# Optimization experiments

Measured on AMD Instinct MI355X. Metric: run time of the kernel, lower is better.

## Reference

```python
import jax, jax.numpy as jnp
import numpy as np

# LIFNode defaults from spikingjelly: decay_input=True, hard reset (v_reset=0.0),
# surrogate = Sigmoid(alpha=4.0).
TAU = 2.0
V_TH = 0.1
V_RESET = 0.0
ALPHA = 4.0  # sigmoid surrogate sharpness

@jax.custom_vjp
def heaviside(x):
    return (x >= 0).astype(x.dtype)

def _hv_fwd(x):
    return heaviside(x), x

def _hv_bwd(x, g):
    s = jax.nn.sigmoid(ALPHA * x)
    return (g * ALPHA * s * (1.0 - s),)

heaviside.defvjp(_hv_fwd, _hv_bwd)

def lif(v, x):
    # charge: v = v + (x - (v - v_reset)) / tau
    v = v + (x - (v - V_RESET)) / TAU
    s = heaviside(v - V_TH)
    # hard reset
    v = (1.0 - s) * v + s * V_RESET
    return v, s

def setup_inputs() -> dict:
    key = jax.random.key(0)
    k0, k1, k2, k3, k4 = jax.random.split(key, 5)
    T, N, I, H = 1024, 32, 1024, 1024
    sx = 1.0 / np.sqrt(I)
    sh = 1.0 / np.sqrt(H)
    return {
        "inputs": jax.random.normal(k0, (T, N, I), jnp.float32),
        "Wx": jax.random.uniform(k1, (4 * H, I), jnp.float32, -sx, sx),
        "bx": jax.random.uniform(k2, (4 * H,), jnp.float32, -sx, sx),
        "Wh": jax.random.uniform(k3, (4 * H, H), jnp.float32, -sh, sh),
        "bh": jax.random.uniform(k4, (4 * H,), jnp.float32, -sh, sh),
    }

def reference(inputs, Wx, bx, Wh, bh):
    T, N, _ = inputs.shape
    H = Wh.shape[1]
    z = jnp.zeros((N, H), inputs.dtype)
    carry0 = (z, z, z, z, z, z, z)  # h, c, v_i, v_f, v_o, v_cs, v_ct

    def step(carry, x_t):
        h, c, vi, vf, vo, vcs, vct = carry
        gates = x_t @ Wx.T + bx + h @ Wh.T + bh  # [N, 4H]
        ig, og, fg, csg = jnp.split(gates, 4, axis=1)  # split order: i, o, f, c_state
        vi, si = lif(vi, ig)
        vf, sf = lif(vf, fg)
        vo, so = lif(vo, og)
        vcs, scs = lif(vcs, csg)
        c = sf * c + si * scs
        vct, sct = lif(vct, c)
        h = so * sct
        return (h, c, vi, vf, vo, vcs, vct), h

    carry, outputs = jax.lax.scan(step, carry0, inputs)
    h_t, c_t = carry[0], carry[1]
    return outputs, (h_t, c_t)
```

## Files before the change

### kernel.cpp

```cpp
#include <hip/hip_runtime.h>


#define NBATCH 32
#define HID    1024
#define FH     4096
#define TK     1024
#define TT     1024
#define TNH    (TT * NBATCH * HID)

__global__ __launch_bounds__(256) void k_zero(double* __restrict__ p, int n) {
    int i = blockIdx.x * 256 + threadIdx.x;
    int stride = gridDim.x * 256;
    for (; i < n; i += stride) p[i] = 0.0;
}

__global__ __launch_bounds__(256) void k_prep(const float* __restrict__ Wh,
                                              double* __restrict__ Whp) {
    __shared__ float tile[64][33];
    int tid = threadIdx.x;
    int jt = blockIdx.x & 63;
    int kt = blockIdx.x >> 6;
    int j0 = jt * 64, k0 = kt * 32;
#pragma unroll
    for (int s = 0; s < 2; ++s) {
        int q = tid * 2 + s;
        int jj = q >> 3, kq = q & 7;
        float4 f = *(const float4*)(Wh + (size_t)(j0 + jj) * TK + k0 + kq * 4);
        tile[jj][kq * 4 + 0] = f.x;
        tile[jj][kq * 4 + 1] = f.y;
        tile[jj][kq * 4 + 2] = f.z;
        tile[jj][kq * 4 + 3] = f.w;
    }
    __syncthreads();
#pragma unroll
    for (int r = 0; r < 8; ++r) {
        int lin = r * 256 + tid;
        int jj2 = lin & 63, kk2 = lin >> 6;
        Whp[(size_t)(k0 + kk2) * FH + j0 + jj2] = (double)tile[jj2][kk2];
    }
}

#define BK 16
__global__ __launch_bounds__(256) void k_xgemm(const float* __restrict__ X,
                                               const float* __restrict__ Wx,
                                               const float* __restrict__ bx,
                                               const float* __restrict__ bh,
                                               double* __restrict__ Gx) {
    __shared__ double Al[BK][130];
    __shared__ double Bl[BK][66];
    int tid = threadIdx.x;
    int j0 = blockIdx.x * 64;
    size_t m0 = (size_t)blockIdx.y * 128;

    double acc[8][4];
#pragma unroll
    for (int r = 0; r < 8; ++r)
#pragma unroll
        for (int c = 0; c < 4; ++c) acc[r][c] = 0.0;

    int mo4 = (tid & 15) * 4;
    int jo4 = (tid >> 4) * 4;
    int mm = tid >> 1, kh = (tid & 1) * 8;
    int jj = tid >> 2, kq = (tid & 3) * 4;

    for (int k0 = 0; k0 < TK; k0 += BK) {
        float4 fa0 = *(const float4*)(X + (m0 + mm) * TK + k0 + kh);
        float4 fa1 = *(const float4*)(X + (m0 + mm) * TK + k0 + kh + 4);
        float4 fb  = *(const float4*)(Wx + (size_t)(j0 + jj) * TK + k0 + kq);
        Al[kh + 0][mm] = fa0.x; Al[kh + 1][mm] = fa0.y;
        Al[kh + 2][mm] = fa0.z; Al[kh + 3][mm] = fa0.w;
        Al[kh + 4][mm] = fa1.x; Al[kh + 5][mm] = fa1.y;
        Al[kh + 6][mm] = fa1.z; Al[kh + 7][mm] = fa1.w;
        Bl[kq + 0][jj] = fb.x; Bl[kq + 1][jj] = fb.y;
        Bl[kq + 2][jj] = fb.z; Bl[kq + 3][jj] = fb.w;
        __syncthreads();
#pragma unroll
        for (int kk = 0; kk < BK; ++kk) {
            double a[8], b[4];
#pragma unroll
            for (int i = 0; i < 4; ++i) {
                a[i]     = Al[kk][mo4 + i];
                a[4 + i] = Al[kk][64 + mo4 + i];
                b[i]     = Bl[kk][jo4 + i];
            }
#pragma unroll
            for (int r = 0; r < 8; ++r)
#pragma unroll
                for (int c = 0; c < 4; ++c) acc[r][c] += a[r] * b[c];
        }
        __syncthreads();
    }

    double bsum[4];
#pragma unroll
    for (int c = 0; c < 4; ++c) {
        int j = j0 + jo4 + c;
        bsum[c] = (double)bx[j] + (double)bh[j];
    }
#pragma unroll
    for (int r = 0; r < 8; ++r) {
        int mloc = (r < 4) ? (mo4 + r) : (64 + mo4 + (r - 4));
        double* dst = Gx + (m0 + mloc) * FH + j0 + jo4;
#pragma unroll
        for (int c = 0; c < 4; ++c) dst[c] = acc[r][c] + bsum[c];
    }
}

__global__ __launch_bounds__(256) void k_rec(const double* __restrict__ Whp,
                                             const double* __restrict__ hprev,
                                             double* __restrict__ part) {
    __shared__ double hlds[NBATCH * 128];
    int tid = threadIdx.x;
    int b = blockIdx.x;
    int jb = b >> 3;
    int ks = b & 7;
    int kbase = ks * 128;
    int j0 = jb * 128 + (tid & 31) * 4;
    int n0 = (tid >> 5) * 4;

#pragma unroll
    for (int r = 0; r < 16; ++r) {
        int lin = r * 256 + tid;
        int n = lin >> 7, kk = lin & 127;
        hlds[lin] = hprev[(size_t)n * HID + kbase + kk];
    }
    __syncthreads();

    double acc[4][4];
#pragma unroll
    for (int a = 0; a < 4; ++a)
#pragma unroll
        for (int c = 0; c < 4; ++c) acc[a][c] = 0.0;

    const double* wp = Whp + (size_t)kbase * FH + j0;
#pragma unroll 2
    for (int kk = 0; kk < 128; ++kk) {
        double w0 = wp[0], w1 = wp[1], w2 = wp[2], w3 = wp[3];
        double h0 = hlds[(n0 + 0) * 128 + kk];
        double h1 = hlds[(n0 + 1) * 128 + kk];
        double h2 = hlds[(n0 + 2) * 128 + kk];
        double h3 = hlds[(n0 + 3) * 128 + kk];
        acc[0][0] += h0 * w0; acc[0][1] += h0 * w1; acc[0][2] += h0 * w2; acc[0][3] += h0 * w3;
        acc[1][0] += h1 * w0; acc[1][1] += h1 * w1; acc[1][2] += h1 * w2; acc[1][3] += h1 * w3;
        acc[2][0] += h2 * w0; acc[2][1] += h2 * w1; acc[2][2] += h2 * w2; acc[2][3] += h2 * w3;
        acc[3][0] += h3 * w0; acc[3][1] += h3 * w1; acc[3][2] += h3 * w2; acc[3][3] += h3 * w3;
        wp += FH;
    }

#pragma unroll
    for (int a = 0; a < 4; ++a) {
        double* dst = part + ((size_t)ks * NBATCH + n0 + a) * FH + j0;
        dst[0] = acc[a][0]; dst[1] = acc[a][1]; dst[2] = acc[a][2]; dst[3] = acc[a][3];
    }
}

__global__ __launch_bounds__(256) void k_lif(const double* __restrict__ Gx,
                                             const double* __restrict__ part,
                                             double* __restrict__ vi_s,
                                             double* __restrict__ vo_s,
                                             double* __restrict__ vf_s,
                                             double* __restrict__ vcs_s,
                                             double* __restrict__ vct_s,
                                             double* __restrict__ c_s,
                                             double* __restrict__ hnext,
                                             float* __restrict__ out,
                                             int t, int tl) {
    int u = blockIdx.x * 256 + threadIdx.x;
    int n = u >> 10, jH = u & 1023;
    size_t base = ((size_t)tl * NBATCH + n) * FH + jH;

    double g[4];
#pragma unroll
    for (int grp = 0; grp < 4; ++grp) {
        double s = Gx[base + grp * HID];
#pragma unroll
        for (int ks = 0; ks < 8; ++ks)
            s += part[((size_t)ks * NBATCH + n) * FH + grp * HID + jH];
        g[grp] = s;
    }

    double v, si, so, sf, scs, sct;

    v = vi_s[u];  v = v + (g[0] - v) * 0.5;
    si = ((v - 0.1) >= 0.0) ? 1.0 : 0.0;  v = (1.0 - si) * v;  vi_s[u] = v;

    v = vf_s[u];  v = v + (g[2] - v) * 0.5;
    sf = ((v - 0.1) >= 0.0) ? 1.0 : 0.0;  v = (1.0 - sf) * v;  vf_s[u] = v;

    v = vo_s[u];  v = v + (g[1] - v) * 0.5;
    so = ((v - 0.1) >= 0.0) ? 1.0 : 0.0;  v = (1.0 - so) * v;  vo_s[u] = v;

    v = vcs_s[u]; v = v + (g[3] - v) * 0.5;
    scs = ((v - 0.1) >= 0.0) ? 1.0 : 0.0; v = (1.0 - scs) * v; vcs_s[u] = v;

    double c = c_s[u];
    c = sf * c + si * scs;
    c_s[u] = c;

    v = vct_s[u]; v = v + (c - v) * 0.5;
    sct = ((v - 0.1) >= 0.0) ? 1.0 : 0.0; v = (1.0 - sct) * v; vct_s[u] = v;

    double h = so * sct;
    hnext[u] = h;
    out[(size_t)t * (NBATCH * HID) + u] = (float)h;
    if (t == TT - 1) {
        out[(size_t)TNH + u] = (float)h;
        out[(size_t)TNH + NBATCH * HID + u] = (float)c;
    }
}

extern "C" void kernel_launch(void* const* d_in, const int* in_sizes, int n_in,
                              void* d_out, int out_size, void* d_ws, size_t ws_size,
                              hipStream_t stream) {
    (void)in_sizes; (void)n_in; (void)out_size;
    const float* X  = (const float*)d_in[0];
    const float* Wx = (const float*)d_in[1];
    const float* bx = (const float*)d_in[2];
    const float* Wh = (const float*)d_in[3];
    const float* bh = (const float*)d_in[4];
    float* out = (float*)d_out;

    double* ws   = (double*)d_ws;
    double* Whp  = ws;
    double* part = Whp + (size_t)TK * FH;
    double* st   = part + (size_t)8 * NBATCH * FH;
    double* vi_s  = st;
    double* vo_s  = vi_s  + 32768;
    double* vf_s  = vo_s  + 32768;
    double* vcs_s = vf_s  + 32768;
    double* vct_s = vcs_s + 32768;
    double* c_s   = vct_s + 32768;
    double* hb0   = c_s   + 32768;
    double* hb1   = hb0   + 32768;
    double* Gx    = hb1   + 32768;

    size_t fixedB = ((size_t)TK * FH + (size_t)8 * NBATCH * FH + (size_t)8 * 32768) * 8;
    int ct = 8;
    for (int cand = 1024; cand >= 8; cand >>= 1) {
        if (fixedB + (size_t)cand * NBATCH * FH * 8 <= ws_size) { ct = cand; break; }
    }
    int nchunk = TT / ct;

    hipLaunchKernelGGL(k_zero, dim3(256), dim3(256), 0, stream, st, 8 * 32768);
    hipLaunchKernelGGL(k_prep, dim3(2048), dim3(256), 0, stream, Wh, Whp);

    for (int c = 0; c < nchunk; ++c) {
        const float* Xc = X + (size_t)c * ct * NBATCH * TK;
        hipLaunchKernelGGL(k_xgemm, dim3(64, (ct * NBATCH) / 128), dim3(256), 0, stream,
                           Xc, Wx, bx, bh, Gx);
        for (int tl = 0; tl < ct; ++tl) {
            int t = c * ct + tl;
            const double* hp = (t & 1) ? hb1 : hb0;
            double* hn = (t & 1) ? hb0 : hb1;
            hipLaunchKernelGGL(k_rec, dim3(256), dim3(256), 0, stream, Whp, hp, part);
            hipLaunchKernelGGL(k_lif, dim3(128), dim3(256), 0, stream, Gx, part,
                               vi_s, vo_s, vf_s, vcs_s, vct_s, c_s, hn, out, t, tl);
        }
    }
}
```

Baseline: 36.44 ms.

## Fuse recurrent GEMM and LIF into persistent cooperative kernel with grid sync

```diff
diff --git a/kernel.cpp b/kernel.cpp
--- a/kernel.cpp
+++ b/kernel.cpp
@@ -1,4 +1,7 @@
 #include <hip/hip_runtime.h>
+#include <hip/hip_cooperative_groups.h>
+
+namespace cg = cooperative_groups;
 
 
 #define NBATCH 32
@@ -8,35 +11,27 @@
 #define TT     1024
 #define TNH    (TT * NBATCH * HID)
 
-__global__ __launch_bounds__(256) void k_zero(double* __restrict__ p, int n) {
-    int i = blockIdx.x * 256 + threadIdx.x;
-    int stride = gridDim.x * 256;
+__global__ __launch_bounds__(256) void k_zero(double* __restrict__ p, long n) {
+    long i = blockIdx.x * 256L + threadIdx.x;
+    long stride = (long)gridDim.x * 256L;
     for (; i < n; i += stride) p[i] = 0.0;
 }
 
-__global__ __launch_bounds__(256) void k_prep(const float* __restrict__ Wh,
-                                              double* __restrict__ Whp) {
-    __shared__ float tile[64][33];
-    int tid = threadIdx.x;
-    int jt = blockIdx.x & 63;
-    int kt = blockIdx.x >> 6;
-    int j0 = jt * 64, k0 = kt * 32;
-#pragma unroll
-    for (int s = 0; s < 2; ++s) {
-        int q = tid * 2 + s;
-        int jj = q >> 3, kq = q & 7;
-        float4 f = *(const float4*)(Wh + (size_t)(j0 + jj) * TK + k0 + kq * 4);
-        tile[jj][kq * 4 + 0] = f.x;
-        tile[jj][kq * 4 + 1] = f.y;
-        tile[jj][kq * 4 + 2] = f.z;
-        tile[jj][kq * 4 + 3] = f.w;
+__global__ __launch_bounds__(256) void k_prep2(const float* __restrict__ Wh,
+                                               double* __restrict__ Whpp) {
+    __shared__ float t[16][1028];
+    int b = blockIdx.x, tid = threadIdx.x;
+    for (int r = 0; r < 16; ++r) {
+        int g = r >> 2, hl = r & 3;
+        const float* src = Wh + (size_t)(g * 1024 + b * 4 + hl) * TK;
+        for (int k = tid; k < TK; k += 256) t[r][k] = src[k];
     }
     __syncthreads();
-#pragma unroll
-    for (int r = 0; r < 8; ++r) {
-        int lin = r * 256 + tid;
-        int jj2 = lin & 63, kk2 = lin >> 6;
-        Whp[(size_t)(k0 + kk2) * FH + j0 + jj2] = (double)tile[jj2][kk2];
+    double* dst = Whpp + (size_t)b * 16384;
+    for (int i = 0; i < 64; ++i) {
+        int lin = i * 256 + tid;
+        int k = lin >> 4, col = lin & 15;
+        dst[lin] = (double)t[col][k];
     }
 }
 
@@ -76,17 +71,17 @@
         __syncthreads();
 #pragma unroll
         for (int kk = 0; kk < BK; ++kk) {
-            double a[8], b[4];
+            double a[8], bb[4];
 #pragma unroll
             for (int i = 0; i < 4; ++i) {
                 a[i]     = Al[kk][mo4 + i];
                 a[4 + i] = Al[kk][64 + mo4 + i];
-                b[i]     = Bl[kk][jo4 + i];
+                bb[i]    = Bl[kk][jo4 + i];
             }
 #pragma unroll
             for (int r = 0; r < 8; ++r)
 #pragma unroll
-                for (int c = 0; c < 4; ++c) acc[r][c] += a[r] * b[c];
+                for (int c = 0; c < 4; ++c) acc[r][c] += a[r] * bb[c];
         }
         __syncthreads();
     }
@@ -106,106 +101,141 @@
     }
 }
 
-__global__ __launch_bounds__(256) void k_rec(const double* __restrict__ Whp,
-                                             const double* __restrict__ hprev,
-                                             double* __restrict__ part) {
-    __shared__ double hlds[NBATCH * 128];
+__global__ __launch_bounds__(512) void k_steps(const double* __restrict__ Whpp,
+                                               double* __restrict__ hg,
+                                               double* __restrict__ stateg,
+                                               const double* __restrict__ Gx,
+                                               float* __restrict__ out,
+                                               int t0, int ct, int gsync) {
+    __shared__ __align__(16) double wlds[2][128 * 16];
+    __shared__ __align__(16) double hlds[2][128 * 32];
+    __shared__ __align__(16) double redbuf[8][512];
+
     int tid = threadIdx.x;
     int b = blockIdx.x;
-    int jb = b >> 3;
-    int ks = b & 7;
-    int kbase = ks * 128;
-    int j0 = jb * 128 + (tid & 31) * 4;
-    int n0 = (tid >> 5) * 4;
-
-#pragma unroll
-    for (int r = 0; r < 16; ++r) {
-        int lin = r * 256 + tid;
-        int n = lin >> 7, kk = lin & 127;
-        hlds[lin] = hprev[(size_t)n * HID + kbase + kk];
-    }
-    __syncthreads();
-
-    double acc[4][4];
-#pragma unroll
-    for (int a = 0; a < 4; ++a)
-#pragma unroll
-        for (int c = 0; c < 4; ++c) acc[a][c] = 0.0;
-
-    const double* wp = Whp + (size_t)kbase * FH + j0;
-#pragma unroll 2
-    for (int kk = 0; kk < 128; ++kk) {
-        double w0 = wp[0], w1 = wp[1], w2 = wp[2], w3 = wp[3];
-        double h0 = hlds[(n0 + 0) * 128 + kk];
-        double h1 = hlds[(n0 + 1) * 128 + kk];
-        double h2 = hlds[(n0 + 2) * 128 + kk];
-        double h3 = hlds[(n0 + 3) * 128 + kk];
-        acc[0][0] += h0 * w0; acc[0][1] += h0 * w1; acc[0][2] += h0 * w2; acc[0][3] += h0 * w3;
-        acc[1][0] += h1 * w0; acc[1][1] += h1 * w1; acc[1][2] += h1 * w2; acc[1][3] += h1 * w3;
-        acc[2][0] += h2 * w0; acc[2][1] += h2 * w1; acc[2][2] += h2 * w2; acc[2][3] += h2 * w3;
-        acc[3][0] += h3 * w0; acc[3][1] += h3 * w1; acc[3][2] += h3 * w2; acc[3][3] += h3 * w3;
-        wp += FH;
-    }
-
-#pragma unroll
-    for (int a = 0; a < 4; ++a) {
-        double* dst = part + ((size_t)ks * NBATCH + n0 + a) * FH + j0;
-        dst[0] = acc[a][0]; dst[1] = acc[a][1]; dst[2] = acc[a][2]; dst[3] = acc[a][3];
-    }
-}
-
-__global__ __launch_bounds__(256) void k_lif(const double* __restrict__ Gx,
-                                             const double* __restrict__ part,
-                                             double* __restrict__ vi_s,
-                                             double* __restrict__ vo_s,
-                                             double* __restrict__ vf_s,
-                                             double* __restrict__ vcs_s,
-                                             double* __restrict__ vct_s,
-                                             double* __restrict__ c_s,
-                                             double* __restrict__ hnext,
-                                             float* __restrict__ out,
-                                             int t, int tl) {
-    int u = blockIdx.x * 256 + threadIdx.x;
-    int n = u >> 10, jH = u & 1023;
-    size_t base = ((size_t)tl * NBATCH + n) * FH + jH;
-
-    double g[4];
-#pragma unroll
-    for (int grp = 0; grp < 4; ++grp) {
-        double s = Gx[base + grp * HID];
-#pragma unroll
-        for (int ks = 0; ks < 8; ++ks)
-            s += part[((size_t)ks * NBATCH + n) * FH + grp * HID + jH];
-        g[grp] = s;
-    }
-
-    double v, si, so, sf, scs, sct;
-
-    v = vi_s[u];  v = v + (g[0] - v) * 0.5;
-    si = ((v - 0.1) >= 0.0) ? 1.0 : 0.0;  v = (1.0 - si) * v;  vi_s[u] = v;
-
-    v = vf_s[u];  v = v + (g[2] - v) * 0.5;
-    sf = ((v - 0.1) >= 0.0) ? 1.0 : 0.0;  v = (1.0 - sf) * v;  vf_s[u] = v;
-
-    v = vo_s[u];  v = v + (g[1] - v) * 0.5;
-    so = ((v - 0.1) >= 0.0) ? 1.0 : 0.0;  v = (1.0 - so) * v;  vo_s[u] = v;
-
-    v = vcs_s[u]; v = v + (g[3] - v) * 0.5;
-    scs = ((v - 0.1) >= 0.0) ? 1.0 : 0.0; v = (1.0 - scs) * v; vcs_s[u] = v;
-
-    double c = c_s[u];
-    c = sf * c + si * scs;
-    c_s[u] = c;
-
-    v = vct_s[u]; v = v + (c - v) * 0.5;
-    sct = ((v - 0.1) >= 0.0) ? 1.0 : 0.0; v = (1.0 - sct) * v; vct_s[u] = v;
-
-    double h = so * sct;
-    hnext[u] = h;
-    out[(size_t)t * (NBATCH * HID) + u] = (float)h;
-    if (t == TT - 1) {
-        out[(size_t)TNH + u] = (float)h;
-        out[(size_t)TNH + NBATCH * HID + u] = (float)c;
+    int wave = tid >> 6, lane = tid & 63;
+    int cp = lane & 7;
+    int ng = lane >> 3;
+    int hl = tid & 3, nl = tid >> 2;
+
+    double vi = 0, vf = 0, vo = 0, vcs = 0, vct = 0, cc = 0;
+    int u = nl * HID + b * 4 + hl;
+    if (tid < 128) {
+        vi  = stateg[u];
+        vf  = stateg[32768 + u];
+        vo  = stateg[65536 + u];
+        vcs = stateg[98304 + u];
+        vct = stateg[131072 + u];
+        cc  = stateg[163840 + u];
+    }
+    const double* wsrc = Whpp + (size_t)b * 16384;
+
+    for (int t = t0; t < t0 + ct; ++t) {
+        const double* hgr = hg + (size_t)(t & 1) * 32768;
+        double*       hgw = hg + (size_t)((t + 1) & 1) * 32768;
+
+        double acc[4][2];
+#pragma unroll
+        for (int a = 0; a < 4; ++a) { acc[a][0] = 0.0; acc[a][1] = 0.0; }
+
+        if (t > 0) {
+            double2 rw0, rw1, rh0, rh1, rh2, rh3;
+            {
+                const double2* gw = (const double2*)wsrc;
+                const double2* gh = (const double2*)hgr;
+                rw0 = gw[tid]; rw1 = gw[512 + tid];
+                rh0 = gh[tid]; rh1 = gh[512 + tid];
+                rh2 = gh[1024 + tid]; rh3 = gh[1536 + tid];
+                double2* dw = (double2*)wlds[0];
+                double2* dh = (double2*)hlds[0];
+                dw[tid] = rw0; dw[512 + tid] = rw1;
+                dh[tid] = rh0; dh[512 + tid] = rh1;
+                dh[1024 + tid] = rh2; dh[1536 + tid] = rh3;
+            }
+            for (int c = 0; c < 8; ++c) {
+                __syncthreads();
+                int buf = c & 1;
+                if (c < 7) {
+                    const double2* gw = (const double2*)(wsrc + (c + 1) * 2048);
+                    const double2* gh = (const double2*)(hgr + (c + 1) * 4096);
+                    rw0 = gw[tid]; rw1 = gw[512 + tid];
+                    rh0 = gh[tid]; rh1 = gh[512 + tid];
+                    rh2 = gh[1024 + tid]; rh3 = gh[1536 + tid];
+                }
+                const double* wb = wlds[buf];
+                const double* hb = hlds[buf];
+#pragma unroll
+                for (int kk = 0; kk < 16; ++kk) {
+                    int k = wave * 16 + kk;
+                    double2 wv  = *(const double2*)&wb[k * 16 + cp * 2];
+                    double2 h01 = *(const double2*)&hb[k * 32 + ng * 4];
+                    double2 h23 = *(const double2*)&hb[k * 32 + ng * 4 + 2];
+                    acc[0][0] += h01.x * wv.x; acc[0][1] += h01.x * wv.y;
+                    acc[1][0] += h01.y * wv.x; acc[1][1] += h01.y * wv.y;
+                    acc[2][0] += h23.x * wv.x; acc[2][1] += h23.x * wv.y;
+                    acc[3][0] += h23.y * wv.x; acc[3][1] += h23.y * wv.y;
+                }
+                if (c < 7) {
+                    int nbuf = buf ^ 1;
+                    double2* dw = (double2*)wlds[nbuf];
+                    double2* dh = (double2*)hlds[nbuf];
+                    dw[tid] = rw0; dw[512 + tid] = rw1;
+                    dh[tid] = rh0; dh[512 + tid] = rh1;
+                    dh[1024 + tid] = rh2; dh[1536 + tid] = rh3;
+                }
+            }
+        }
+
+#pragma unroll
+        for (int a = 0; a < 4; ++a) {
+            int n = ng * 4 + a;
+            redbuf[wave][(cp * 2 + 0) * 32 + n] = acc[a][0];
+            redbuf[wave][(cp * 2 + 1) * 32 + n] = acc[a][1];
+        }
+        __syncthreads();
+
+        if (tid < 128) {
+            int tl = t - t0;
+            double g[4];
+#pragma unroll
+            for (int gi = 0; gi < 4; ++gi) {
+                int col = gi * 4 + hl;
+                double s = Gx[((size_t)tl * NBATCH + nl) * FH + gi * 1024 + b * 4 + hl];
+#pragma unroll
+                for (int w = 0; w < 8; ++w) s += redbuf[w][col * 32 + nl];
+                g[gi] = s;
+            }
+            double v, si, sf, so, scs, sct;
+            v = vi;  v = v + (g[0] - v) * 0.5;
+            si  = ((v - 0.1) >= 0.0) ? 1.0 : 0.0;  vi  = (1.0 - si)  * v;
+            v = vf;  v = v + (g[2] - v) * 0.5;
+            sf  = ((v - 0.1) >= 0.0) ? 1.0 : 0.0;  vf  = (1.0 - sf)  * v;
+            v = vo;  v = v + (g[1] - v) * 0.5;
+            so  = ((v - 0.1) >= 0.0) ? 1.0 : 0.0;  vo  = (1.0 - so)  * v;
+            v = vcs; v = v + (g[3] - v) * 0.5;
+            scs = ((v - 0.1) >= 0.0) ? 1.0 : 0.0;  vcs = (1.0 - scs) * v;
+            cc = sf * cc + si * scs;
+            v = vct; v = v + (cc - v) * 0.5;
+            sct = ((v - 0.1) >= 0.0) ? 1.0 : 0.0;  vct = (1.0 - sct) * v;
+            double h = so * sct;
+
+            hgw[(b * 4 + hl) * 32 + nl] = h;
+            out[(size_t)t * (NBATCH * HID) + nl * HID + b * 4 + hl] = (float)h;
+            if (t == TT - 1) {
+                out[(size_t)TNH + nl * HID + b * 4 + hl] = (float)h;
+                out[(size_t)TNH + NBATCH * HID + nl * HID + b * 4 + hl] = (float)cc;
+            }
+        }
+        if (gsync) cg::this_grid().sync();
+    }
+
+    if (tid < 128) {
+        stateg[u]          = vi;
+        stateg[32768 + u]  = vf;
+        stateg[65536 + u]  = vo;
+        stateg[98304 + u]  = vcs;
+        stateg[131072 + u] = vct;
+        stateg[163840 + u] = cc;
     }
 }
 
@@ -220,41 +250,45 @@
     const float* bh = (const float*)d_in[4];
     float* out = (float*)d_out;
 
-    double* ws   = (double*)d_ws;
-    double* Whp  = ws;
-    double* part = Whp + (size_t)TK * FH;
-    double* st   = part + (size_t)8 * NBATCH * FH;
-    double* vi_s  = st;
-    double* vo_s  = vi_s  + 32768;
-    double* vf_s  = vo_s  + 32768;
-    double* vcs_s = vf_s  + 32768;
-    double* vct_s = vcs_s + 32768;
-    double* c_s   = vct_s + 32768;
-    double* hb0   = c_s   + 32768;
-    double* hb1   = hb0   + 32768;
-    double* Gx    = hb1   + 32768;
-
-    size_t fixedB = ((size_t)TK * FH + (size_t)8 * NBATCH * FH + (size_t)8 * 32768) * 8;
+    double* ws     = (double*)d_ws;
+    double* Whpp   = ws;
+    double* stateg = Whpp + 4194304;
+    double* hg     = stateg + 196608;
+    double* Gx     = hg + 65536;
+
+    size_t fixedB = (4194304ULL + 196608ULL + 65536ULL) * 8;
     int ct = 8;
     for (int cand = 1024; cand >= 8; cand >>= 1) {
         if (fixedB + (size_t)cand * NBATCH * FH * 8 <= ws_size) { ct = cand; break; }
     }
     int nchunk = TT / ct;
 
-    hipLaunchKernelGGL(k_zero, dim3(256), dim3(256), 0, stream, st, 8 * 32768);
-    hipLaunchKernelGGL(k_prep, dim3(2048), dim3(256), 0, stream, Wh, Whp);
+    hipLaunchKernelGGL(k_zero, dim3(64), dim3(256), 0, stream, stateg, 196608L);
+    hipLaunchKernelGGL(k_prep2, dim3(256), dim3(256), 0, stream, Wh, Whpp);
 
     for (int c = 0; c < nchunk; ++c) {
         const float* Xc = X + (size_t)c * ct * NBATCH * TK;
         hipLaunchKernelGGL(k_xgemm, dim3(64, (ct * NBATCH) / 128), dim3(256), 0, stream,
                            Xc, Wx, bx, bh, Gx);
-        for (int tl = 0; tl < ct; ++tl) {
-            int t = c * ct + tl;
-            const double* hp = (t & 1) ? hb1 : hb0;
-            double* hn = (t & 1) ? hb0 : hb1;
-            hipLaunchKernelGGL(k_rec, dim3(256), dim3(256), 0, stream, Whp, hp, part);
-            hipLaunchKernelGGL(k_lif, dim3(128), dim3(256), 0, stream, Gx, part,
-                               vi_s, vo_s, vf_s, vcs_s, vct_s, c_s, hn, out, t, tl);
-        }
-    }
-}
+        int t0 = c * ct;
+        const double* whpp_a = Whpp;
+        double* hg_a = hg;
+        double* st_a = stateg;
+        const double* gx_a = Gx;
+        float* out_a = out;
+        int one = 1;
+        void* args[] = { (void*)&whpp_a, (void*)&hg_a, (void*)&st_a,
+                         (void*)&gx_a, (void*)&out_a, (void*)&t0, (void*)&ct,
+                         (void*)&one };
+        hipError_t e = hipLaunchCooperativeKernel((const void*)k_steps, dim3(256),
+                                                  dim3(512), args, 0, stream);
+        if (e != hipSuccess) {
+            for (int tl = 0; tl < ct; ++tl) {
+                int t = t0 + tl;
+                hipLaunchKernelGGL(k_steps, dim3(256), dim3(512), 0, stream,
+                                   Whpp, hg, stateg, Gx + (size_t)tl * NBATCH * FH,
+                                   out, t, 1, 0);
+            }
+        }
+    }
+}
```

Result: slower. 55.14 ms (+51.3%).
